# Kernel tuning notes

Hardware: AMD Instinct MI355X
Metric: run time of the kernel (lower is better)

Reference implementation:

```python
import jax, jax.numpy as jnp
import numpy as np

B, T, H, N = 4, 2048, 1024, 16
DT_MIN, DT_MAX = 1e-3, 1e-1
A_INIT_MIN, A_INIT_MAX = 0.5, 2.0


def _inv_softplus(x):
    # log(exp(x) - 1), numerically stable
    return x + jnp.log(-jnp.expm1(-x))


def setup_inputs() -> dict:
    key = jax.random.key(0)
    kx, ka, kb, kc, kw, kdt = jax.random.split(key, 6)
    x = jax.random.normal(kx, (B, T, H), dtype=jnp.float32)
    A_log = jax.random.uniform(ka, (H, N), minval=np.log(A_INIT_MIN), maxval=np.log(A_INIT_MAX), dtype=jnp.float32)
    B_mat = 0.02 * jax.random.normal(kb, (H, N), dtype=jnp.float32)
    C_mat = 0.02 * jax.random.normal(kc, (H, N), dtype=jnp.float32)
    D_vec = jnp.ones((H,), dtype=jnp.float32)
    W_dt = 0.02 * jax.random.normal(kw, (H, H), dtype=jnp.float32)
    b_dt = _inv_softplus(jax.random.uniform(kdt, (H,), minval=DT_MIN, maxval=DT_MAX, dtype=jnp.float32))
    return {"x": x, "A_log": A_log, "B_mat": B_mat, "C_mat": C_mat, "D_vec": D_vec, "W_dt": W_dt, "b_dt": b_dt}


def reference(x, A_log, B_mat, C_mat, D_vec, W_dt, b_dt):
    # in_proj is Identity since input_size == hidden_size
    u = x  # (B, T, H)
    A = -jnp.exp(A_log)  # (H, N)
    # dt for all timesteps at once: softplus(u @ W_dt^T + b_dt) -> (B, T, H)
    dt = jax.nn.softplus(jnp.einsum('bth,gh->btg', u, W_dt) + b_dt)
    state0 = jnp.zeros((u.shape[0], A_log.shape[0], A_log.shape[1]), dtype=u.dtype)

    def step(state, inp):
        dt_t, u_t = inp  # (B, H), (B, H)
        dtA = dt_t[..., None]  # (B, H, 1)
        A_bar = jnp.exp(dtA * A)                       # (B, H, N)
        state = A_bar * state + (dtA * B_mat) * u_t[..., None]
        y_t = jnp.einsum('bhn,hn->bh', state, C_mat) + D_vec * u_t
        return state, y_t

    # scan over time axis
    state_final, ys = jax.lax.scan(step, state0, (dt.transpose(1, 0, 2), u.transpose(1, 0, 2)))
    out = ys.transpose(1, 0, 2)  # (B, T, H)
    return out, state_final
```

## Files before the change

### kernel.cpp

```cpp
#include <hip/hip_runtime.h>
#include <stdint.h>

#define BB 4
#define TT 2048
#define HH 1024
#define NN 16
#define KK 1024
#define GG 1024
#define MM (BB*TT)
#define NCHUNK 16
#define TC (TT/NCHUNK)

#if __has_builtin(__builtin_amdgcn_exp2f)
#define FAST_EXP2(x) __builtin_amdgcn_exp2f(x)
#else
#define FAST_EXP2(x) __expf((x) * 0.6931471805599453f)
#endif
#define EXPSCALE 1.4426950408889634f

typedef __attribute__((ext_vector_type(8))) short short8;
typedef __attribute__((ext_vector_type(4))) float f32x4;

__device__ __forceinline__ unsigned short f2bf(float f) {
  union { float f; unsigned u; } a; a.f = f;
  unsigned u = a.u;
  u += 0x7fffu + ((u >> 16) & 1u);
  return (unsigned short)(u >> 16);
}

__global__ __launch_bounds__(256) void cvt_f32_bf16(const float* __restrict__ src,
                                                    unsigned short* __restrict__ dst, int n4) {
  int i = blockIdx.x * blockDim.x + threadIdx.x;
  if (i >= n4) return;
  float4 a = ((const float4*)src)[i];
  ushort4 o;
  o.x = f2bf(a.x); o.y = f2bf(a.y); o.z = f2bf(a.z); o.w = f2bf(a.w);
  ((ushort4*)dst)[i] = o;
}

__global__ __launch_bounds__(256) void gemm_dt(const unsigned short* __restrict__ xb,
                                               const unsigned short* __restrict__ wb,
                                               const float* __restrict__ b_dt,
                                               float* __restrict__ dtT) {
  __shared__ short lsA[128 * 32];
  __shared__ short lsB[64 * 32];
  const int tid  = threadIdx.x;
  const int w    = tid >> 6;
  const int lane = tid & 63;
  const int m0 = blockIdx.x * 128;
  const int g0 = blockIdx.y * 64;

  const int ea  = w * 1024 + lane * 8;
  const int am0 = ea >> 5,         ak0 = ea & 31;
  const int am1 = (ea + 512) >> 5, ak1 = (ea + 512) & 31;
  const int eb  = w * 512 + lane * 8;
  const int bg0 = eb >> 5,         bk0 = eb & 31;
  const unsigned short* gA0 = xb + (size_t)(m0 + am0) * KK + ak0;
  const unsigned short* gA1 = xb + (size_t)(m0 + am1) * KK + ak1;
  const unsigned short* gB0 = wb + (size_t)(g0 + bg0) * KK + bk0;
  short* lA0 = lsA + w * 1024;
  short* lB0 = lsB + w * 512;

  const int wm   = (w >> 1) * 64;
  const int wg   = (w & 1) * 32;
  const int lrow = lane & 15;
  const int lq   = lane >> 4;

  f32x4 acc[4][2];
  const f32x4 zero = {0.f, 0.f, 0.f, 0.f};
#pragma unroll
  for (int i = 0; i < 4; ++i)
#pragma unroll
    for (int j = 0; j < 2; ++j) acc[i][j] = zero;

  for (int kt = 0; kt < KK / 32; ++kt) {
    const int ko = kt * 32;
    __builtin_amdgcn_global_load_lds((__attribute__((address_space(1))) void*)(gA0 + ko),
                                     (__attribute__((address_space(3))) void*)(lA0), 16, 0, 0);
    __builtin_amdgcn_global_load_lds((__attribute__((address_space(1))) void*)(gA1 + ko),
                                     (__attribute__((address_space(3))) void*)(lA0 + 512), 16, 0, 0);
    __builtin_amdgcn_global_load_lds((__attribute__((address_space(1))) void*)(gB0 + ko),
                                     (__attribute__((address_space(3))) void*)(lB0), 16, 0, 0);
    __syncthreads();

    short8 af[4], bfr[2];
#pragma unroll
    for (int mi = 0; mi < 4; ++mi)
      af[mi] = *(const short8*)&lsA[(wm + mi * 16 + lrow) * 32 + lq * 8];
#pragma unroll
    for (int ni = 0; ni < 2; ++ni)
      bfr[ni] = *(const short8*)&lsB[(wg + ni * 16 + lrow) * 32 + lq * 8];
#pragma unroll
    for (int mi = 0; mi < 4; ++mi)
#pragma unroll
      for (int ni = 0; ni < 2; ++ni)
        acc[mi][ni] = __builtin_amdgcn_mfma_f32_16x16x32_bf16(af[mi], bfr[ni], acc[mi][ni], 0, 0, 0);
    __syncthreads();
  }

  const int b  = m0 >> 11;
  const int tb = (m0 & (TT - 1)) + wm + lq * 4;
#pragma unroll
  for (int mi = 0; mi < 4; ++mi)
#pragma unroll
    for (int ni = 0; ni < 2; ++ni) {
      const int gcol = g0 + wg + ni * 16 + lrow;
      const float bias = b_dt[gcol];
      f32x4 sp;
#pragma unroll
      for (int r = 0; r < 4; ++r) {
        float z = acc[mi][ni][r] + bias;
        sp[r] = fmaxf(z, 0.f) + __logf(1.f + __expf(-fabsf(z)));
      }
      *(f32x4*)&dtT[((size_t)b * HH + gcol) * TT + tb + mi * 16] = sp;
    }
}

__device__ __forceinline__ float reduce16(float (&v)[16], int n16) {
#pragma unroll
  for (int i = 0; i < 8; ++i) {
    float lo = v[i], hi = v[i + 8];
    float snd = (n16 & 8) ? lo : hi;
    float rcv = __shfl_xor(snd, 8);
    v[i] = ((n16 & 8) ? hi : lo) + rcv;
  }
#pragma unroll
  for (int i = 0; i < 4; ++i) {
    float lo = v[i], hi = v[i + 4];
    float snd = (n16 & 4) ? lo : hi;
    float rcv = __shfl_xor(snd, 4);
    v[i] = ((n16 & 4) ? hi : lo) + rcv;
  }
#pragma unroll
  for (int i = 0; i < 2; ++i) {
    float lo = v[i], hi = v[i + 2];
    float snd = (n16 & 2) ? lo : hi;
    float rcv = __shfl_xor(snd, 2);
    v[i] = ((n16 & 2) ? hi : lo) + rcv;
  }
  float lo = v[0], hi = v[1];
  float snd = (n16 & 1) ? lo : hi;
  float rcv = __shfl_xor(snd, 1);
  return ((n16 & 1) ? hi : lo) + rcv;
}

__device__ __forceinline__ float bcast16(float ureg, int idxbyte) {
  union { float f; int i; } a, r; a.f = ureg;
  r.i = __builtin_amdgcn_ds_bpermute(idxbyte, a.i);
  return r.f;
}

__device__ __forceinline__ void step16_p1(float& s, float& sd, const f32x4* dd, float ureg,
                                          int idxb, float Ae) {
#pragma unroll
  for (int q = 0; q < 4; ++q) {
#pragma unroll
    for (int k = 0; k < 4; ++k) {
      const int kk = q * 4 + k;
      float dtv = dd[q][k];
      float uv  = bcast16(ureg, idxb + kk * 4);
      float ab  = FAST_EXP2(dtv * Ae);
      s = fmaf(ab, s, dtv * uv);
      sd += dtv;
    }
  }
}

__device__ __forceinline__ void step16_p3(float& s, const f32x4* dd, float ureg, int idxb,
                                          float Ae, float Cb, float Dv,
                                          int n16, float* __restrict__ yp) {
  float v[16];
#pragma unroll
  for (int q = 0; q < 4; ++q) {
#pragma unroll
    for (int k = 0; k < 4; ++k) {
      const int kk = q * 4 + k;
      float dtv = dd[q][k];
      float uv  = bcast16(ureg, idxb + kk * 4);
      float ab  = FAST_EXP2(dtv * Ae);
      s = fmaf(ab, s, dtv * uv);
      v[kk] = Cb * s;
    }
  }
  float y = reduce16(v, n16);
  *yp = fmaf(Dv, ureg, y);
}

__global__ __launch_bounds__(256) void ssm_phase1(const float* __restrict__ x,
                                                  const float* __restrict__ dtT,
                                                  const float* __restrict__ A_log,
                                                  float* __restrict__ sloc,
                                                  float* __restrict__ decay) {
  const int tid = threadIdx.x;
  const int g   = tid >> 4;
  const int n16 = tid & 15;
  const int bid = blockIdx.x;
  const int ht  = bid & 63;
  const int b   = (bid >> 6) & 3;
  const int c   = bid >> 8;
  const int h   = (ht << 4) + g;
  const int lane = tid & 63;
  const int tl   = lane & 15;
  const int idxb = (lane & 48) << 2;

  const float Aneg = -__expf(A_log[h * NN + n16]);
  const float Ae   = Aneg * EXPSCALE;

  const f32x4* dp4 = (const f32x4*)(dtT + ((size_t)b * HH + h) * TT + c * TC);
  const float* up  = x + (size_t)b * TT * HH + (size_t)(c * TC + tl) * HH + h;

  float s = 0.f, sd = 0.f;
  f32x4 d0[4], d1[4];
  float u0, u1;
#pragma unroll
  for (int i = 0; i < 4; ++i) d0[i] = dp4[i];
  u0 = up[0];

#pragma unroll 1
  for (int j = 0; j < TC / 16; j += 2) {
#pragma unroll
    for (int i = 0; i < 4; ++i) d1[i] = dp4[(j + 1) * 4 + i];
    u1 = up[(size_t)(j + 1) * 16 * HH];
    step16_p1(s, sd, d0, u0, idxb, Ae);
    if (j + 2 < TC / 16) {
#pragma unroll
      for (int i = 0; i < 4; ++i) d0[i] = dp4[(j + 2) * 4 + i];
      u0 = up[(size_t)(j + 2) * 16 * HH];
    }
    step16_p1(s, sd, d1, u1, idxb, Ae);
  }

  const size_t idx = (((size_t)c * BB + b) * HH + h) * NN + n16;
  sloc[idx]  = s;
  decay[idx] = FAST_EXP2(Ae * sd);
}

__global__ __launch_bounds__(256) void ssm_phase2(float* __restrict__ sloc,
                                                  const float* __restrict__ decay,
                                                  const float* __restrict__ Bm_,
                                                  float* __restrict__ stateOut) {
  const int id = blockIdx.x * 256 + threadIdx.x;
  float carry = 0.f;
#pragma unroll
  for (int c = 0; c < NCHUNK; ++c) {
    const size_t idx = (size_t)c * (BB * HH * NN) + id;
    const float sl = sloc[idx];
    const float dc = decay[idx];
    sloc[idx] = carry;
    carry = fmaf(dc, carry, sl);
  }
  stateOut[id] = Bm_[id & (HH * NN - 1)] * carry;
}

__global__ __launch_bounds__(256) void ssm_phase3(const float* __restrict__ x,
                                                  const float* __restrict__ dtT,
                                                  const float* __restrict__ A_log,
                                                  const float* __restrict__ Bm_,
                                                  const float* __restrict__ Cm_,
                                                  const float* __restrict__ Dv_,
                                                  const float* __restrict__ carryBuf,
                                                  float* __restrict__ out) {
  const int tid = threadIdx.x;
  const int g   = tid >> 4;
  const int n16 = tid & 15;
  const int bid = blockIdx.x;
  const int ht  = bid & 63;
  const int b   = (bid >> 6) & 3;
  const int c   = bid >> 8;
  const int h   = (ht << 4) + g;
  const int lane = tid & 63;
  const int tl   = lane & 15;
  const int idxb = (lane & 48) << 2;

  const float Aneg = -__expf(A_log[h * NN + n16]);
  const float Ae   = Aneg * EXPSCALE;
  const float Cb   = Cm_[h * NN + n16] * Bm_[h * NN + n16];
  const float Dv   = Dv_[h];

  const f32x4* dp4 = (const f32x4*)(dtT + ((size_t)b * HH + h) * TT + c * TC);
  const float* up  = x + (size_t)b * TT * HH + (size_t)(c * TC + tl) * HH + h;
  float* yp = out + (size_t)b * TT * HH + (size_t)(c * TC + n16) * HH + h;

  float s = carryBuf[(((size_t)c * BB + b) * HH + h) * NN + n16];
  f32x4 d0[4], d1[4];
  float u0, u1;
#pragma unroll
  for (int i = 0; i < 4; ++i) d0[i] = dp4[i];
  u0 = up[0];

#pragma unroll 1
  for (int j = 0; j < TC / 16; j += 2) {
#pragma unroll
    for (int i = 0; i < 4; ++i) d1[i] = dp4[(j + 1) * 4 + i];
    u1 = up[(size_t)(j + 1) * 16 * HH];
    step16_p3(s, d0, u0, idxb, Ae, Cb, Dv, n16, yp);
    yp += 16 * HH;
    if (j + 2 < TC / 16) {
#pragma unroll
      for (int i = 0; i < 4; ++i) d0[i] = dp4[(j + 2) * 4 + i];
      u0 = up[(size_t)(j + 2) * 16 * HH];
    }
    step16_p3(s, d1, u1, idxb, Ae, Cb, Dv, n16, yp);
    yp += 16 * HH;
  }
}

extern "C" void kernel_launch(void* const* d_in, const int* in_sizes, int n_in,
                              void* d_out, int out_size, void* d_ws, size_t ws_size,
                              hipStream_t stream) {
  const float* x     = (const float*)d_in[0];
  const float* A_log = (const float*)d_in[1];
  const float* B_mat = (const float*)d_in[2];
  const float* C_mat = (const float*)d_in[3];
  const float* D_vec = (const float*)d_in[4];
  const float* W_dt  = (const float*)d_in[5];
  const float* b_dt  = (const float*)d_in[6];
  float* out = (float*)d_out;

  char* ws = (char*)d_ws;
  unsigned short* xb  = (unsigned short*)(ws);
  unsigned short* wb  = (unsigned short*)(ws + 16777216);
  float*          dtT = (float*)(ws + 18874368);
  float*          sloc  = (float*)(ws);
  float*          decay = (float*)(ws + 4194304);
  float* stateOut = out + (size_t)BB * TT * HH;

  cvt_f32_bf16<<<(MM * KK / 4 + 255) / 256, 256, 0, stream>>>(x, xb, MM * KK / 4);
  cvt_f32_bf16<<<(GG * KK / 4 + 255) / 256, 256, 0, stream>>>(W_dt, wb, GG * KK / 4);
  gemm_dt<<<dim3(MM / 128, GG / 64), 256, 0, stream>>>(xb, wb, b_dt, dtT);

  const int nblk = BB * (HH / 16) * NCHUNK;
  ssm_phase1<<<nblk, 256, 0, stream>>>(x, dtT, A_log, sloc, decay);
  ssm_phase2<<<(BB * HH * NN) / 256, 256, 0, stream>>>(sloc, decay, B_mat, stateOut);
  ssm_phase3<<<nblk, 256, 0, stream>>>(x, dtT, A_log, B_mat, C_mat, D_vec, sloc, out);
}
```

Before: 209.6 us.

## Store dt and dt*u as bf16 transposed from GEMM epilogue, merge conversions

The GEMM epilogue now stages the matching x tile in shared memory and writes both softplus(dt) and dt*u as transposed bf16 arrays. The scan phases read these packed bf16 streams instead of fp32 dt plus strided x loads with cross-lane bpermute broadcasts. Phase1 no longer reads x at all. The two fp32-to-bf16 conversion launches are merged into one. This halves dt traffic and removes the bpermute work, at the cost of bf16 rounding on dt and dt*u in the recurrence, plus extra epilogue loads and LDS use in the GEMM.

```diff
diff --git a/kernel.cpp b/kernel.cpp
--- a/kernel.cpp
+++ b/kernel.cpp
@@ -20,6 +20,7 @@
 
 typedef __attribute__((ext_vector_type(8))) short short8;
 typedef __attribute__((ext_vector_type(4))) float f32x4;
+typedef __attribute__((ext_vector_type(4))) unsigned int u32x4;
 
 __device__ __forceinline__ unsigned short f2bf(float f) {
   union { float f; unsigned u; } a; a.f = f;
@@ -27,23 +28,37 @@
   u += 0x7fffu + ((u >> 16) & 1u);
   return (unsigned short)(u >> 16);
 }
-
-__global__ __launch_bounds__(256) void cvt_f32_bf16(const float* __restrict__ src,
-                                                    unsigned short* __restrict__ dst, int n4) {
+__device__ __forceinline__ float bflo(unsigned w) {
+  union { unsigned u; float f; } c; c.u = w << 16; return c.f;
+}
+__device__ __forceinline__ float bfhi(unsigned w) {
+  union { unsigned u; float f; } c; c.u = w & 0xffff0000u; return c.f;
+}
+
+__global__ __launch_bounds__(256) void cvt_all(const float* __restrict__ x,
+                                               const float* __restrict__ w,
+                                               unsigned short* __restrict__ xb,
+                                               unsigned short* __restrict__ wb) {
   int i = blockIdx.x * blockDim.x + threadIdx.x;
-  if (i >= n4) return;
-  float4 a = ((const float4*)src)[i];
+  const int nx = MM * KK / 4;
+  const float* src; unsigned short* dst; int j;
+  if (i < nx) { src = x; dst = xb; j = i; }
+  else        { src = w; dst = wb; j = i - nx; if (j >= GG * KK / 4) return; }
+  float4 a = ((const float4*)src)[j];
   ushort4 o;
   o.x = f2bf(a.x); o.y = f2bf(a.y); o.z = f2bf(a.z); o.w = f2bf(a.w);
-  ((ushort4*)dst)[i] = o;
+  ((ushort4*)dst)[j] = o;
 }
 
 __global__ __launch_bounds__(256) void gemm_dt(const unsigned short* __restrict__ xb,
                                                const unsigned short* __restrict__ wb,
+                                               const float* __restrict__ xf,
                                                const float* __restrict__ b_dt,
-                                               float* __restrict__ dtT) {
-  __shared__ short lsA[128 * 32];
-  __shared__ short lsB[64 * 32];
+                                               unsigned short* __restrict__ dtT,
+                                               unsigned short* __restrict__ dtuT) {
+  __shared__ float uls[128 * 64];
+  short* lsA = (short*)uls;
+  short* lsB = lsA + 128 * 32;
   const int tid  = threadIdx.x;
   const int w    = tid >> 6;
   const int lane = tid & 63;
@@ -98,6 +113,21 @@
     __syncthreads();
   }
 
+  float4 ur[8];
+#pragma unroll
+  for (int i = 0; i < 8; ++i) {
+    const int idx = tid + 256 * i;
+    const int row = idx >> 4, c4 = idx & 15;
+    ur[i] = *(const float4*)&xf[(size_t)(m0 + row) * HH + g0 + c4 * 4];
+  }
+#pragma unroll
+  for (int i = 0; i < 8; ++i) {
+    const int idx = tid + 256 * i;
+    const int row = idx >> 4, c4 = idx & 15;
+    *(float4*)&uls[row * 64 + c4 * 4] = ur[i];
+  }
+  __syncthreads();
+
   const int b  = m0 >> 11;
   const int tb = (m0 & (TT - 1)) + wm + lq * 4;
 #pragma unroll
@@ -106,13 +136,18 @@
     for (int ni = 0; ni < 2; ++ni) {
       const int gcol = g0 + wg + ni * 16 + lrow;
       const float bias = b_dt[gcol];
-      f32x4 sp;
+      ushort4 dt4, du4;
 #pragma unroll
       for (int r = 0; r < 4; ++r) {
         float z = acc[mi][ni][r] + bias;
-        sp[r] = fmaxf(z, 0.f) + __logf(1.f + __expf(-fabsf(z)));
+        float sp = fmaxf(z, 0.f) + __logf(1.f + __expf(-fabsf(z)));
+        float u  = uls[(wm + mi * 16 + lq * 4 + r) * 64 + wg + ni * 16 + lrow];
+        ((unsigned short*)&dt4)[r] = f2bf(sp);
+        ((unsigned short*)&du4)[r] = f2bf(sp * u);
       }
-      *(f32x4*)&dtT[((size_t)b * HH + gcol) * TT + tb + mi * 16] = sp;
+      const size_t o = ((size_t)b * HH + gcol) * TT + tb + mi * 16;
+      *(ushort4*)&dtT[o]  = dt4;
+      *(ushort4*)&dtuT[o] = du4;
     }
 }
 
@@ -144,50 +179,45 @@
   return ((n16 & 1) ? hi : lo) + rcv;
 }
 
-__device__ __forceinline__ float bcast16(float ureg, int idxbyte) {
-  union { float f; int i; } a, r; a.f = ureg;
-  r.i = __builtin_amdgcn_ds_bpermute(idxbyte, a.i);
-  return r.f;
-}
-
-__device__ __forceinline__ void step16_p1(float& s, float& sd, const f32x4* dd, float ureg,
-                                          int idxb, float Ae) {
-#pragma unroll
-  for (int q = 0; q < 4; ++q) {
-#pragma unroll
-    for (int k = 0; k < 4; ++k) {
-      const int kk = q * 4 + k;
-      float dtv = dd[q][k];
-      float uv  = bcast16(ureg, idxb + kk * 4);
-      float ab  = FAST_EXP2(dtv * Ae);
-      s = fmaf(ab, s, dtv * uv);
-      sd += dtv;
-    }
-  }
-}
-
-__device__ __forceinline__ void step16_p3(float& s, const f32x4* dd, float ureg, int idxb,
-                                          float Ae, float Cb, float Dv,
-                                          int n16, float* __restrict__ yp) {
+__device__ __forceinline__ void group16_p1(float& s, float& sd,
+                                           const u32x4* D, const u32x4* G, float Ae) {
+#pragma unroll
+  for (int q = 0; q < 2; ++q)
+#pragma unroll
+    for (int e = 0; e < 4; ++e) {
+      const unsigned wd = D[q][e], wg_ = G[q][e];
+      float d0 = bflo(wd), g0v = bflo(wg_);
+      s = fmaf(FAST_EXP2(d0 * Ae), s, g0v);
+      sd += d0;
+      float d1 = bfhi(wd), g1v = bfhi(wg_);
+      s = fmaf(FAST_EXP2(d1 * Ae), s, g1v);
+      sd += d1;
+    }
+}
+
+__device__ __forceinline__ void group16_p3(float& s, const u32x4* D, const u32x4* G,
+                                           float ureg, float Ae, float Cb, float Dv,
+                                           int n16, float* __restrict__ yp) {
   float v[16];
 #pragma unroll
-  for (int q = 0; q < 4; ++q) {
-#pragma unroll
-    for (int k = 0; k < 4; ++k) {
-      const int kk = q * 4 + k;
-      float dtv = dd[q][k];
-      float uv  = bcast16(ureg, idxb + kk * 4);
-      float ab  = FAST_EXP2(dtv * Ae);
-      s = fmaf(ab, s, dtv * uv);
+  for (int q = 0; q < 2; ++q)
+#pragma unroll
+    for (int e = 0; e < 4; ++e) {
+      const int kk = q * 8 + e * 2;
+      const unsigned wd = D[q][e], wg_ = G[q][e];
+      float d0 = bflo(wd), g0v = bflo(wg_);
+      s = fmaf(FAST_EXP2(d0 * Ae), s, g0v);
       v[kk] = Cb * s;
-    }
-  }
+      float d1 = bfhi(wd), g1v = bfhi(wg_);
+      s = fmaf(FAST_EXP2(d1 * Ae), s, g1v);
+      v[kk + 1] = Cb * s;
+    }
   float y = reduce16(v, n16);
   *yp = fmaf(Dv, ureg, y);
 }
 
-__global__ __launch_bounds__(256) void ssm_phase1(const float* __restrict__ x,
-                                                  const float* __restrict__ dtT,
+__global__ __launch_bounds__(256) void ssm_phase1(const unsigned short* __restrict__ dtT,
+                                                  const unsigned short* __restrict__ dtuT,
                                                   const float* __restrict__ A_log,
                                                   float* __restrict__ sloc,
                                                   float* __restrict__ decay) {
@@ -199,35 +229,26 @@
   const int b   = (bid >> 6) & 3;
   const int c   = bid >> 8;
   const int h   = (ht << 4) + g;
-  const int lane = tid & 63;
-  const int tl   = lane & 15;
-  const int idxb = (lane & 48) << 2;
-
-  const float Aneg = -__expf(A_log[h * NN + n16]);
-  const float Ae   = Aneg * EXPSCALE;
-
-  const f32x4* dp4 = (const f32x4*)(dtT + ((size_t)b * HH + h) * TT + c * TC);
-  const float* up  = x + (size_t)b * TT * HH + (size_t)(c * TC + tl) * HH + h;
+
+  const float Ae = -__expf(A_log[h * NN + n16]) * EXPSCALE;
+
+  const u32x4* dp = (const u32x4*)(dtT  + ((size_t)b * HH + h) * TT + c * TC);
+  const u32x4* gp = (const u32x4*)(dtuT + ((size_t)b * HH + h) * TT + c * TC);
 
   float s = 0.f, sd = 0.f;
-  f32x4 d0[4], d1[4];
-  float u0, u1;
-#pragma unroll
-  for (int i = 0; i < 4; ++i) d0[i] = dp4[i];
-  u0 = up[0];
+  u32x4 D0[2], G0[2], D1[2], G1[2];
+  D0[0] = dp[0]; D0[1] = dp[1]; G0[0] = gp[0]; G0[1] = gp[1];
 
 #pragma unroll 1
   for (int j = 0; j < TC / 16; j += 2) {
-#pragma unroll
-    for (int i = 0; i < 4; ++i) d1[i] = dp4[(j + 1) * 4 + i];
-    u1 = up[(size_t)(j + 1) * 16 * HH];
-    step16_p1(s, sd, d0, u0, idxb, Ae);
+    D1[0] = dp[(j + 1) * 2];     D1[1] = dp[(j + 1) * 2 + 1];
+    G1[0] = gp[(j + 1) * 2];     G1[1] = gp[(j + 1) * 2 + 1];
+    group16_p1(s, sd, D0, G0, Ae);
     if (j + 2 < TC / 16) {
-#pragma unroll
-      for (int i = 0; i < 4; ++i) d0[i] = dp4[(j + 2) * 4 + i];
-      u0 = up[(size_t)(j + 2) * 16 * HH];
-    }
-    step16_p1(s, sd, d1, u1, idxb, Ae);
+      D0[0] = dp[(j + 2) * 2];   D0[1] = dp[(j + 2) * 2 + 1];
+      G0[0] = gp[(j + 2) * 2];   G0[1] = gp[(j + 2) * 2 + 1];
+    }
+    group16_p1(s, sd, D1, G1, Ae);
   }
 
   const size_t idx = (((size_t)c * BB + b) * HH + h) * NN + n16;
@@ -253,7 +274,8 @@
 }
 
 __global__ __launch_bounds__(256) void ssm_phase3(const float* __restrict__ x,
-                                                  const float* __restrict__ dtT,
+                                                  const unsigned short* __restrict__ dtT,
+                                                  const unsigned short* __restrict__ dtuT,
                                                   const float* __restrict__ A_log,
                                                   const float* __restrict__ Bm_,
                                                   const float* __restrict__ Cm_,
@@ -268,39 +290,35 @@
   const int b   = (bid >> 6) & 3;
   const int c   = bid >> 8;
   const int h   = (ht << 4) + g;
-  const int lane = tid & 63;
-  const int tl   = lane & 15;
-  const int idxb = (lane & 48) << 2;
-
-  const float Aneg = -__expf(A_log[h * NN + n16]);
-  const float Ae   = Aneg * EXPSCALE;
-  const float Cb   = Cm_[h * NN + n16] * Bm_[h * NN + n16];
-  const float Dv   = Dv_[h];
-
-  const f32x4* dp4 = (const f32x4*)(dtT + ((size_t)b * HH + h) * TT + c * TC);
-  const float* up  = x + (size_t)b * TT * HH + (size_t)(c * TC + tl) * HH + h;
+
+  const float Ae = -__expf(A_log[h * NN + n16]) * EXPSCALE;
+  const float Cb = Cm_[h * NN + n16] * Bm_[h * NN + n16];
+  const float Dv = Dv_[h];
+
+  const u32x4* dp = (const u32x4*)(dtT  + ((size_t)b * HH + h) * TT + c * TC);
+  const u32x4* gp = (const u32x4*)(dtuT + ((size_t)b * HH + h) * TT + c * TC);
+  const float* up = x + (size_t)b * TT * HH + (size_t)(c * TC + n16) * HH + h;
   float* yp = out + (size_t)b * TT * HH + (size_t)(c * TC + n16) * HH + h;
 
   float s = carryBuf[(((size_t)c * BB + b) * HH + h) * NN + n16];
-  f32x4 d0[4], d1[4];
+  u32x4 D0[2], G0[2], D1[2], G1[2];
   float u0, u1;
-#pragma unroll
-  for (int i = 0; i < 4; ++i) d0[i] = dp4[i];
+  D0[0] = dp[0]; D0[1] = dp[1]; G0[0] = gp[0]; G0[1] = gp[1];
   u0 = up[0];
 
 #pragma unroll 1
   for (int j = 0; j < TC / 16; j += 2) {
-#pragma unroll
-    for (int i = 0; i < 4; ++i) d1[i] = dp4[(j + 1) * 4 + i];
+    D1[0] = dp[(j + 1) * 2];     D1[1] = dp[(j + 1) * 2 + 1];
+    G1[0] = gp[(j + 1) * 2];     G1[1] = gp[(j + 1) * 2 + 1];
     u1 = up[(size_t)(j + 1) * 16 * HH];
-    step16_p3(s, d0, u0, idxb, Ae, Cb, Dv, n16, yp);
+    group16_p3(s, D0, G0, u0, Ae, Cb, Dv, n16, yp);
     yp += 16 * HH;
     if (j + 2 < TC / 16) {
-#pragma unroll
-      for (int i = 0; i < 4; ++i) d0[i] = dp4[(j + 2) * 4 + i];
+      D0[0] = dp[(j + 2) * 2];   D0[1] = dp[(j + 2) * 2 + 1];
+      G0[0] = gp[(j + 2) * 2];   G0[1] = gp[(j + 2) * 2 + 1];
       u0 = up[(size_t)(j + 2) * 16 * HH];
     }
-    step16_p3(s, d1, u1, idxb, Ae, Cb, Dv, n16, yp);
+    group16_p3(s, D1, G1, u1, Ae, Cb, Dv, n16, yp);
     yp += 16 * HH;
   }
 }
@@ -318,19 +336,19 @@
   float* out = (float*)d_out;
 
   char* ws = (char*)d_ws;
-  unsigned short* xb  = (unsigned short*)(ws);
-  unsigned short* wb  = (unsigned short*)(ws + 16777216);
-  float*          dtT = (float*)(ws + 18874368);
+  unsigned short* xb   = (unsigned short*)(ws);
+  unsigned short* wb   = (unsigned short*)(ws + 16777216);
+  unsigned short* dtT  = (unsigned short*)(ws + 18874368);
+  unsigned short* dtuT = (unsigned short*)(ws + 35651584);
   float*          sloc  = (float*)(ws);
   float*          decay = (float*)(ws + 4194304);
   float* stateOut = out + (size_t)BB * TT * HH;
 
-  cvt_f32_bf16<<<(MM * KK / 4 + 255) / 256, 256, 0, stream>>>(x, xb, MM * KK / 4);
-  cvt_f32_bf16<<<(GG * KK / 4 + 255) / 256, 256, 0, stream>>>(W_dt, wb, GG * KK / 4);
-  gemm_dt<<<dim3(MM / 128, GG / 64), 256, 0, stream>>>(xb, wb, b_dt, dtT);
+  cvt_all<<<(MM * KK / 4 + GG * KK / 4 + 255) / 256, 256, 0, stream>>>(x, W_dt, xb, wb);
+  gemm_dt<<<dim3(MM / 128, GG / 64), 256, 0, stream>>>(xb, wb, x, b_dt, dtT, dtuT);
 
   const int nblk = BB * (HH / 16) * NCHUNK;
-  ssm_phase1<<<nblk, 256, 0, stream>>>(x, dtT, A_log, sloc, decay);
+  ssm_phase1<<<nblk, 256, 0, stream>>>(dtT, dtuT, A_log, sloc, decay);
   ssm_phase2<<<(BB * HH * NN) / 256, 256, 0, stream>>>(sloc, decay, B_mat, stateOut);
-  ssm_phase3<<<nblk, 256, 0, stream>>>(x, dtT, A_log, B_mat, C_mat, D_vec, sloc, out);
-}
+  ssm_phase3<<<nblk, 256, 0, stream>>>(x, dtT, dtuT, A_log, B_mat, C_mat, D_vec, sloc, out);
+}
```

Measured after the change: 211.1 us. No clear change (+0.7%).
